# Kernel optimization log

Measured on AMD Instinct MI355X. Metric: run time of the kernel, lower is better.

## Reference

```python
import jax, jax.numpy as jnp
import numpy as np

V, E, H, B, S, T = 32000, 512, 1024, 64, 128, 65

def setup_inputs() -> dict:
    key = jax.random.key(0)
    ks = jax.random.split(key, 10)
    f = lambda k, shape, s=1.0: jax.random.normal(k, shape, jnp.float32) * s
    return {
        "tgt_token_ids": jax.random.randint(ks[0], (T, B), 0, V),
        "enc_hidden": f(ks[1], (B, S, 2 * H)),
        "enc_mask": jnp.zeros((B, S), jnp.int32),  # 1 = masked (pad)
        "dec_init_hidden": f(ks[2], (B, H)),
        "dec_init_cell": f(ks[3], (B, H)),
        "embedding": f(ks[4], (V, E), 0.02),
        "W_ih": f(ks[5], (4 * H, E + H), 0.02),
        "W_hh": f(ks[6], (4 * H, H), 0.02),
        "b_ih": jnp.zeros((4 * H,), jnp.float32),
        "b_hh": jnp.zeros((4 * H,), jnp.float32),
        "W_att": f(ks[7], (H, 2 * H), 0.02),
        "W_comb": f(ks[8], (H, 3 * H), 0.02),
    }


def reference(tgt_token_ids, enc_hidden, enc_mask, dec_init_hidden, dec_init_cell,
              embedding, W_ih, W_hh, b_ih, b_hh, W_att, W_comb):
    mask = enc_mask.astype(bool)
    # enc_hiddens_proj = attention(enc_hidden): [B,S,2H] @ [H,2H].T -> [B,S,H]
    enc_proj = jnp.einsum('bsd,hd->bsh', enc_hidden, W_att)
    y = embedding[tgt_token_ids[:-1]]  # [T-1, B, E]
    # NOTE: faithful to the source, dec_init_state is fed to step() at EVERY
    # timestep (the updated LSTM state is discarded); only o_prev recurs.
    hh_term = dec_init_hidden @ W_hh.T + b_ih + b_hh  # [B, 4H], constant across steps
    c0 = dec_init_cell

    def step(o_prev, y_t):
        ybar = jnp.concatenate([y_t, o_prev], axis=1)        # [B, E+H]
        gates = ybar @ W_ih.T + hh_term                      # [B, 4H]
        i, f, g, o = jnp.split(gates, 4, axis=1)
        c = jax.nn.sigmoid(f) * c0 + jax.nn.sigmoid(i) * jnp.tanh(g)
        h = jax.nn.sigmoid(o) * jnp.tanh(c)                  # dec_hidden [B, H]
        e = jnp.einsum('bsh,bh->bs', enc_proj, h)            # scores [B, S]
        e = jnp.where(mask, -jnp.inf, e)
        alpha = jax.nn.softmax(e, axis=1)
        a = jnp.einsum('bs,bsd->bd', alpha, enc_hidden)      # context [B, 2H]
        U = jnp.concatenate([h, a], axis=1)                  # [B, 3H]
        O = jnp.tanh(U @ W_comb.T)                           # [B, H] (dropout = identity, eval)
        return O, O

    o0 = jnp.zeros_like(dec_init_hidden)
    _, outs = jax.lax.scan(step, o0, y)                      # [T-1, B, H]
    return outs
```

## Files before the change

kernel.cpp:

```cpp
#include <hip/hip_runtime.h>
#include <hip/hip_bf16.h>
#include <math.h>

#define BATCH 64
#define SRC   128
#define HID   1024
#define EMB   512
#define NT    64
#define G4    4096

__device__ __forceinline__ float sigmoidf_(float x){ return 1.0f/(1.0f+expf(-x)); }

template<int AMODE>
__launch_bounds__(256, 2)
__global__ void skinny_gemm(const float* __restrict__ A, int lda,
                            const int* __restrict__ toks, const float* __restrict__ emb,
                            const float* __restrict__ W, int ldw,
                            float* __restrict__ partial, int N, int Kchunk){
  const int nc = blockIdx.x;
  const int kc = blockIdx.y;
  const int kbase = kc * Kchunk;
  const int tid = threadIdx.x;
  __shared__ float As[16][68];
  __shared__ float Bs[16][132];
  const int wave = tid >> 6, lane = tid & 63;
  const int lm = lane & 7, ln = lane >> 3;
  const int nwave = nc*128 + wave*32;
  float acc[8][4] = {};
  const int arow = tid >> 2, akc = (tid & 3) * 4;
  for (int k0 = 0; k0 < Kchunk; k0 += 16){
    int kg = kbase + k0 + akc;
    float4 av;
    if (AMODE == 1){
      if (kg < EMB) av = *(const float4*)(emb + (size_t)toks[arow]*EMB + kg);
      else          av = *(const float4*)(A + (size_t)arow*lda + (kg - EMB));
    } else {
      av = *(const float4*)(A + (size_t)arow*lda + kg);
    }
    As[akc+0][arow]=av.x; As[akc+1][arow]=av.y; As[akc+2][arow]=av.z; As[akc+3][arow]=av.w;
    #pragma unroll
    for (int r = 0; r < 2; ++r){
      int idx = tid + r*256;
      int nrow = idx >> 2, bkc = (idx & 3) * 4;
      float4 wv = *(const float4*)(W + (size_t)(nc*128 + nrow)*ldw + kbase + k0 + bkc);
      Bs[bkc+0][nrow]=wv.x; Bs[bkc+1][nrow]=wv.y; Bs[bkc+2][nrow]=wv.z; Bs[bkc+3][nrow]=wv.w;
    }
    __syncthreads();
    #pragma unroll
    for (int k = 0; k < 16; ++k){
      float4 alo = *(const float4*)&As[k][lm*8];
      float4 ahi = *(const float4*)&As[k][lm*8+4];
      float4 b4  = *(const float4*)&Bs[k][wave*32 + ln*4];
      float am[8] = {alo.x,alo.y,alo.z,alo.w,ahi.x,ahi.y,ahi.z,ahi.w};
      float bn[4] = {b4.x,b4.y,b4.z,b4.w};
      #pragma unroll
      for (int i=0;i<8;++i)
        #pragma unroll
        for (int j=0;j<4;++j)
          acc[i][j] += am[i]*bn[j];
    }
    __syncthreads();
  }
  for (int i=0;i<8;++i){
    int m = lm*8+i;
    float4 v = make_float4(acc[i][0],acc[i][1],acc[i][2],acc[i][3]);
    *(float4*)(partial + ((size_t)(kc*64 + m))*N + nwave + ln*4) = v;
  }
}

__launch_bounds__(256, 2)
__global__ void big_gemm128(const float* __restrict__ A, int lda,
                            const float* __restrict__ W, int ldw,
                            float* __restrict__ C, int N, int K){
  const int n0 = blockIdx.x * 128;
  const int m0 = blockIdx.y * 128;
  const int tid = threadIdx.x;
  __shared__ float As[16][132];
  __shared__ float Bs[16][132];
  const int wave = tid >> 6, lane = tid & 63;
  const int wm = wave >> 1, wn = wave & 1;
  const int lm = lane & 7, ln = lane >> 3;
  float acc[8][8] = {};
  for (int k0 = 0; k0 < K; k0 += 16){
    #pragma unroll
    for (int r = 0; r < 2; ++r){
      int idx = tid + r*256;
      int row = idx >> 2, kq = (idx & 3) * 4;
      float4 av = *(const float4*)(A + (size_t)(m0+row)*lda + k0 + kq);
      As[kq+0][row]=av.x; As[kq+1][row]=av.y; As[kq+2][row]=av.z; As[kq+3][row]=av.w;
      float4 wv = *(const float4*)(W + (size_t)(n0+row)*ldw + k0 + kq);
      Bs[kq+0][row]=wv.x; Bs[kq+1][row]=wv.y; Bs[kq+2][row]=wv.z; Bs[kq+3][row]=wv.w;
    }
    __syncthreads();
    #pragma unroll
    for (int k = 0; k < 16; ++k){
      float4 a0 = *(const float4*)&As[k][wm*64 + lm*8];
      float4 a1 = *(const float4*)&As[k][wm*64 + lm*8 + 4];
      float4 b0 = *(const float4*)&Bs[k][wn*64 + ln*8];
      float4 b1 = *(const float4*)&Bs[k][wn*64 + ln*8 + 4];
      float am[8] = {a0.x,a0.y,a0.z,a0.w,a1.x,a1.y,a1.z,a1.w};
      float bn[8] = {b0.x,b0.y,b0.z,b0.w,b1.x,b1.y,b1.z,b1.w};
      #pragma unroll
      for (int i=0;i<8;++i)
        #pragma unroll
        for (int j=0;j<8;++j)
          acc[i][j] += am[i]*bn[j];
    }
    __syncthreads();
  }
  for (int i=0;i<8;++i){
    int m = m0 + wm*64 + lm*8 + i;
    float* cp = C + (size_t)m*N + n0 + wn*64 + ln*8;
    *(float4*)cp     = make_float4(acc[i][0],acc[i][1],acc[i][2],acc[i][3]);
    *(float4*)(cp+4) = make_float4(acc[i][4],acc[i][5],acc[i][6],acc[i][7]);
  }
}

__global__ void hh_reduce_kernel(const float* __restrict__ partial,
                                 const float* __restrict__ b_ih, const float* __restrict__ b_hh,
                                 float* __restrict__ hh_term){
  int g = blockIdx.x*512 + threadIdx.x;
  int n = g & 4095;
  int b = g >> 12;
  float s = b_ih[n] + b_hh[n];
  #pragma unroll
  for (int kc=0; kc<8; ++kc) s += partial[((size_t)(kc*64+b))*G4 + n];
  hh_term[g] = s;
}

__global__ void h_e_kernel(const float* __restrict__ partial_g, const float* __restrict__ hh_term,
                           const float* __restrict__ c0, const float* __restrict__ enc_proj,
                           float* __restrict__ hbuf, float* __restrict__ e_part){
  const int b = blockIdx.x, ch = blockIdx.y;
  const int tid = threadIdx.x;
  __shared__ float hs[256];
  const int j = ch*256 + tid;
  float gate[4];
  #pragma unroll
  for (int q=0;q<4;++q){
    int n = q*HID + j;
    float s = hh_term[b*G4 + n];
    #pragma unroll
    for (int kc=0;kc<8;++kc) s += partial_g[((size_t)(kc*64+b))*G4 + n];
    gate[q]=s;
  }
  float c = sigmoidf_(gate[1])*c0[b*HID+j] + sigmoidf_(gate[0])*tanhf(gate[2]);
  float h = sigmoidf_(gate[3])*tanhf(c);
  hs[tid] = h;
  hbuf[b*HID + j] = h;
  __syncthreads();
  const int wave = tid>>6, lane = tid&63;
  float4 hv = *(const float4*)&hs[lane*4];
  for (int s = wave; s < SRC; s += 4){
    const float* ep = enc_proj + ((size_t)b*SRC + s)*HID + ch*256;
    float4 v = *(const float4*)(ep + lane*4);
    float sum = v.x*hv.x + v.y*hv.y + v.z*hv.z + v.w*hv.w;
    #pragma unroll
    for (int off=32; off; off>>=1) sum += __shfl_down(sum, off);
    if (lane==0) e_part[(b*4 + ch)*SRC + s] = sum;
  }
}

__global__ void soft_comb_kernel(const float* __restrict__ e_part, const int* __restrict__ enc_mask,
                                 const float* __restrict__ encW, const float* __restrict__ partial_c,
                                 float* __restrict__ Obuf, float* __restrict__ out, int t){
  const int b = blockIdx.x, ch = blockIdx.y;
  const int tid = threadIdx.x;
  __shared__ float als[SRC];
  __shared__ float red[SRC];
  float ev = 0.f; bool msk = false;
  if (tid < SRC){
    ev = e_part[(b*4+0)*SRC+tid] + e_part[(b*4+1)*SRC+tid]
       + e_part[(b*4+2)*SRC+tid] + e_part[(b*4+3)*SRC+tid];
    msk = (enc_mask[b*SRC+tid] != 0);
    red[tid] = msk ? -1e30f : ev;
  }
  __syncthreads();
  for (int off=64; off>=1; off>>=1){ if (tid<off) red[tid]=fmaxf(red[tid],red[tid+off]); __syncthreads(); }
  float mval = red[0]; __syncthreads();
  float p = (tid<SRC && !msk) ? expf(ev-mval) : 0.f;
  if (tid<SRC) red[tid]=p;
  __syncthreads();
  for (int off=64; off>=1; off>>=1){ if (tid<off) red[tid]+=red[tid+off]; __syncthreads(); }
  if (tid<SRC) als[tid] = p/red[0];
  __syncthreads();
  const int j = ch*256 + tid;
  const float* ew = encW + (size_t)b*SRC*HID + j;
  float acc = 0.f;
  #pragma unroll 8
  for (int s=0;s<SRC;++s) acc += als[s]*ew[(size_t)s*HID];
  #pragma unroll
  for (int kc=0;kc<16;++kc) acc += partial_c[((size_t)(kc*64+b))*HID + j];
  float v = tanhf(acc);
  Obuf[b*HID+j] = v;
  out[(size_t)t*BATCH*HID + b*HID + j] = v;
}

__global__ void zero_kernel(float* __restrict__ p, int n){
  int i = blockIdx.x*256 + threadIdx.x;
  if (i < n) p[i] = 0.f;
}

extern "C" void kernel_launch(void* const* d_in, const int* in_sizes, int n_in,
                              void* d_out, int out_size, void* d_ws, size_t ws_size,
                              hipStream_t stream) {
  const int*   tgt        = (const int*)d_in[0];
  const float* enc_hidden = (const float*)d_in[1];
  const int*   enc_mask   = (const int*)d_in[2];
  const float* dih        = (const float*)d_in[3];
  const float* dic        = (const float*)d_in[4];
  const float* emb        = (const float*)d_in[5];
  const float* W_ih       = (const float*)d_in[6];
  const float* W_hh       = (const float*)d_in[7];
  const float* b_ih       = (const float*)d_in[8];
  const float* b_hh       = (const float*)d_in[9];
  const float* W_att      = (const float*)d_in[10];
  const float* W_comb     = (const float*)d_in[11];
  float* out = (float*)d_out;

  float* ws        = (float*)d_ws;
  float* enc_proj  = ws;
  float* encW      = enc_proj + 8388608;
  float* partial_g = encW + 8388608;
  float* partial_c = partial_g + 2097152;
  float* hh_term   = partial_c + 1048576;
  float* hbuf      = hh_term + 262144;
  float* e_part    = hbuf + 65536;
  float* Obuf      = e_part + 32768;

  big_gemm128<<<dim3(8,64), 256, 0, stream>>>(enc_hidden, 2048, W_att, 2048, enc_proj, HID, 2048);
  big_gemm128<<<dim3(8,64), 256, 0, stream>>>(enc_hidden, 2048, W_comb + HID, 3072, encW, HID, 2048);
  skinny_gemm<0><<<dim3(32,8), 256, 0, stream>>>(dih, HID, nullptr, nullptr, W_hh, HID, partial_g, G4, 128);
  hh_reduce_kernel<<<dim3(512), 512, 0, stream>>>(partial_g, b_ih, b_hh, hh_term);
  zero_kernel<<<dim3(256), 256, 0, stream>>>(Obuf, BATCH*HID);

  for (int t = 0; t < NT; ++t){
    skinny_gemm<1><<<dim3(32,8), 256, 0, stream>>>(Obuf, HID, tgt + t*BATCH, emb, W_ih, 1536, partial_g, G4, 192);
    h_e_kernel<<<dim3(64,4), 256, 0, stream>>>(partial_g, hh_term, dic, enc_proj, hbuf, e_part);
    skinny_gemm<0><<<dim3(8,16), 256, 0, stream>>>(hbuf, HID, nullptr, nullptr, W_comb, 3072, partial_c, HID, 64);
    soft_comb_kernel<<<dim3(64,4), 256, 0, stream>>>(e_part, enc_mask, encW, partial_c, Obuf, out, t);
  }
}
```

Before: 5.166 ms.

## Replace per-timestep kernel launches with a persistent decoder using grid barriers

The 64-step loop of four kernels per step becomes one persistent kernel of 256 blocks. Each block keeps its slice of W_ih and W_comb resident in shared memory and steps through time, separated by software grid barriers built on atomics. The aim is to remove launch overhead and the repeated re-reading of weights from global memory on every step. It risks deadlock if the 256 blocks are not all co-resident, since each uses a large shared memory allocation, and it adds barrier latency and a split-softmax combine.

```diff
diff --git a/kernel.cpp b/kernel.cpp
--- a/kernel.cpp
+++ b/kernel.cpp
@@ -128,77 +128,232 @@
   hh_term[g] = s;
 }
 
-__global__ void h_e_kernel(const float* __restrict__ partial_g, const float* __restrict__ hh_term,
-                           const float* __restrict__ c0, const float* __restrict__ enc_proj,
-                           float* __restrict__ hbuf, float* __restrict__ e_part){
-  const int b = blockIdx.x, ch = blockIdx.y;
-  const int tid = threadIdx.x;
-  __shared__ float hs[256];
-  const int j = ch*256 + tid;
-  float gate[4];
-  #pragma unroll
-  for (int q=0;q<4;++q){
-    int n = q*HID + j;
-    float s = hh_term[b*G4 + n];
-    #pragma unroll
-    for (int kc=0;kc<8;++kc) s += partial_g[((size_t)(kc*64+b))*G4 + n];
-    gate[q]=s;
-  }
-  float c = sigmoidf_(gate[1])*c0[b*HID+j] + sigmoidf_(gate[0])*tanhf(gate[2]);
-  float h = sigmoidf_(gate[3])*tanhf(c);
-  hs[tid] = h;
-  hbuf[b*HID + j] = h;
+__global__ void init_kernel(float* __restrict__ Obuf, unsigned* __restrict__ bar){
+  int i = blockIdx.x*512 + threadIdx.x;
+  if (i < BATCH*HID) Obuf[i] = 0.f;
+  if (i < 4) bar[i] = 0u;
+}
+
+__device__ __forceinline__ void grid_barrier(unsigned* bar, unsigned nblocks){
   __syncthreads();
-  const int wave = tid>>6, lane = tid&63;
-  float4 hv = *(const float4*)&hs[lane*4];
-  for (int s = wave; s < SRC; s += 4){
-    const float* ep = enc_proj + ((size_t)b*SRC + s)*HID + ch*256;
-    float4 v = *(const float4*)(ep + lane*4);
-    float sum = v.x*hv.x + v.y*hv.y + v.z*hv.z + v.w*hv.w;
-    #pragma unroll
-    for (int off=32; off; off>>=1) sum += __shfl_down(sum, off);
-    if (lane==0) e_part[(b*4 + ch)*SRC + s] = sum;
-  }
-}
-
-__global__ void soft_comb_kernel(const float* __restrict__ e_part, const int* __restrict__ enc_mask,
-                                 const float* __restrict__ encW, const float* __restrict__ partial_c,
-                                 float* __restrict__ Obuf, float* __restrict__ out, int t){
-  const int b = blockIdx.x, ch = blockIdx.y;
-  const int tid = threadIdx.x;
-  __shared__ float als[SRC];
-  __shared__ float red[SRC];
-  float ev = 0.f; bool msk = false;
-  if (tid < SRC){
-    ev = e_part[(b*4+0)*SRC+tid] + e_part[(b*4+1)*SRC+tid]
-       + e_part[(b*4+2)*SRC+tid] + e_part[(b*4+3)*SRC+tid];
-    msk = (enc_mask[b*SRC+tid] != 0);
-    red[tid] = msk ? -1e30f : ev;
+  if (threadIdx.x == 0){
+    __threadfence();
+    unsigned g = __hip_atomic_load(&bar[1], __ATOMIC_ACQUIRE, __HIP_MEMORY_SCOPE_AGENT);
+    unsigned old = __hip_atomic_fetch_add(&bar[0], 1u, __ATOMIC_ACQ_REL, __HIP_MEMORY_SCOPE_AGENT);
+    if (old == nblocks - 1u){
+      __hip_atomic_store(&bar[0], 0u, __ATOMIC_RELAXED, __HIP_MEMORY_SCOPE_AGENT);
+      __threadfence();
+      __hip_atomic_fetch_add(&bar[1], 1u, __ATOMIC_ACQ_REL, __HIP_MEMORY_SCOPE_AGENT);
+    } else {
+      while (__hip_atomic_load(&bar[1], __ATOMIC_ACQUIRE, __HIP_MEMORY_SCOPE_AGENT) == g)
+        __builtin_amdgcn_s_sleep(2);
+    }
+    __threadfence();
   }
   __syncthreads();
-  for (int off=64; off>=1; off>>=1){ if (tid<off) red[tid]=fmaxf(red[tid],red[tid+off]); __syncthreads(); }
-  float mval = red[0]; __syncthreads();
-  float p = (tid<SRC && !msk) ? expf(ev-mval) : 0.f;
-  if (tid<SRC) red[tid]=p;
+}
+
+__global__ __launch_bounds__(512, 1)
+void decoder_persistent(const int* __restrict__ tgt, const int* __restrict__ enc_mask,
+                        const float* __restrict__ dic, const float* __restrict__ emb,
+                        const float* __restrict__ W_ih, const float* __restrict__ W_comb,
+                        const float* __restrict__ hh_term, const float* __restrict__ enc_proj,
+                        const float* __restrict__ encW,
+                        float* __restrict__ e_g, float* __restrict__ emax_g, float* __restrict__ esum_g,
+                        float* __restrict__ combh, float* __restrict__ hbuf,
+                        float* __restrict__ Obuf, float* __restrict__ out,
+                        unsigned* __restrict__ bar){
+  const int blk = blockIdx.x, tid = threadIdx.x;
+  const int wave = tid >> 6, lane = tid & 63;
+  const int bg = lane >> 2, rg = lane & 3;
+  const int j0 = blk * 4;
+
+  __shared__ float Wg[1536*16];
+  __shared__ float Wc[1024*4];
+  __shared__ float scratch[8704];
+  __shared__ int   toks[64];
+  __shared__ float e_loc[32];
+  __shared__ float al_s[SRC];
+  __shared__ float redp[512];
+
+  for (int rr = 0; rr < 16; ++rr){
+    int row = (rr & 3) * 1024 + j0 + (rr >> 2);
+    for (int k = tid; k < 1536; k += 512) Wg[k*16 + rr] = W_ih[(size_t)row*1536 + k];
+  }
+  for (int j = 0; j < 4; ++j){
+    int n = j0 + j;
+    for (int k = tid; k < 1024; k += 512) Wc[k*4 + j] = W_comb[(size_t)n*3072 + k];
+  }
   __syncthreads();
-  for (int off=64; off>=1; off>>=1){ if (tid<off) red[tid]+=red[tid+off]; __syncthreads(); }
-  if (tid<SRC) als[tid] = p/red[0];
-  __syncthreads();
-  const int j = ch*256 + tid;
-  const float* ew = encW + (size_t)b*SRC*HID + j;
-  float acc = 0.f;
-  #pragma unroll 8
-  for (int s=0;s<SRC;++s) acc += als[s]*ew[(size_t)s*HID];
-  #pragma unroll
-  for (int kc=0;kc<16;++kc) acc += partial_c[((size_t)(kc*64+b))*HID + j];
-  float v = tanhf(acc);
-  Obuf[b*HID+j] = v;
-  out[(size_t)t*BATCH*HID + b*HID + j] = v;
-}
-
-__global__ void zero_kernel(float* __restrict__ p, int n){
-  int i = blockIdx.x*256 + threadIdx.x;
-  if (i < n) p[i] = 0.f;
+
+  for (int t = 0; t < NT; ++t){
+    if (tid < 64) toks[tid] = tgt[t*BATCH + tid];
+    __syncthreads();
+    float acc[4][4] = {};
+    for (int c = 0; c < 12; ++c){
+      {
+        int b = tid & 63, kq = tid >> 6;
+        #pragma unroll
+        for (int i = 0; i < 4; ++i){
+          int kg = c*128 + kq*16 + i*4;
+          float4 v;
+          if (kg < EMB) v = *(const float4*)(emb + (size_t)toks[b]*EMB + kg);
+          else          v = *(const float4*)(Obuf + b*HID + (kg - EMB));
+          int kb = kq*16 + i*4;
+          scratch[(kb+0)*68 + b] = v.x;
+          scratch[(kb+1)*68 + b] = v.y;
+          scratch[(kb+2)*68 + b] = v.z;
+          scratch[(kb+3)*68 + b] = v.w;
+        }
+      }
+      __syncthreads();
+      #pragma unroll
+      for (int kk = 0; kk < 16; ++kk){
+        int k = wave*16 + kk;
+        float4 yb = *(const float4*)&scratch[k*68 + bg*4];
+        float4 wv = *(const float4*)&Wg[(c*128 + k)*16 + rg*4];
+        float ym[4] = {yb.x, yb.y, yb.z, yb.w};
+        float wn[4] = {wv.x, wv.y, wv.z, wv.w};
+        #pragma unroll
+        for (int i = 0; i < 4; ++i)
+          #pragma unroll
+          for (int j = 0; j < 4; ++j)
+            acc[i][j] += ym[i] * wn[j];
+      }
+      __syncthreads();
+    }
+    #pragma unroll
+    for (int i = 0; i < 4; ++i)
+      #pragma unroll
+      for (int j = 0; j < 4; ++j)
+        scratch[wave*1024 + (rg*4 + j)*64 + bg*4 + i] = acc[i][j];
+    __syncthreads();
+    if (tid < 256){
+      int b = tid & 63, jj = tid >> 6;
+      float g4[4];
+      #pragma unroll
+      for (int g = 0; g < 4; ++g){
+        float s = hh_term[b*G4 + g*1024 + j0 + jj];
+        #pragma unroll
+        for (int w = 0; w < 8; ++w) s += scratch[w*1024 + (jj*4 + g)*64 + b];
+        g4[g] = s;
+      }
+      float c_ = sigmoidf_(g4[1]) * dic[b*HID + j0 + jj] + sigmoidf_(g4[0]) * tanhf(g4[2]);
+      hbuf[b*HID + j0 + jj] = sigmoidf_(g4[3]) * tanhf(c_);
+    }
+    grid_barrier(bar, 256);
+
+    {
+      const int b = blk >> 2, sg = blk & 3;
+      for (int i = tid; i < HID; i += 512) scratch[i] = hbuf[b*HID + i];
+      __syncthreads();
+      #pragma unroll
+      for (int q = 0; q < 4; ++q){
+        int s = sg*32 + wave*4 + q;
+        const float* ep = enc_proj + ((size_t)(b*SRC + s))*HID;
+        float sum = 0.f;
+        #pragma unroll
+        for (int m = 0; m < 4; ++m){
+          float4 v  = *(const float4*)(ep + m*256 + lane*4);
+          float4 hv = *(const float4*)&scratch[m*256 + lane*4];
+          sum += v.x*hv.x + v.y*hv.y + v.z*hv.z + v.w*hv.w;
+        }
+        #pragma unroll
+        for (int off = 32; off; off >>= 1) sum += __shfl_down(sum, off);
+        if (lane == 0) e_loc[wave*4 + q] = sum;
+      }
+      __syncthreads();
+      if (wave == 0){
+        int sl = lane & 31;
+        int s = sg*32 + sl;
+        bool valid = lane < 32;
+        bool msk = valid ? (enc_mask[b*SRC + s] != 0) : true;
+        float ev = (valid && !msk) ? e_loc[sl] : -1e30f;
+        if (valid) e_g[b*SRC + s] = ev;
+        float mv = ev;
+        #pragma unroll
+        for (int off = 32; off; off >>= 1) mv = fmaxf(mv, __shfl_down(mv, off));
+        mv = __shfl(mv, 0);
+        float p = (valid && !msk) ? expf(ev - mv) : 0.f;
+        float ps = p;
+        #pragma unroll
+        for (int off = 32; off; off >>= 1) ps += __shfl_down(ps, off);
+        if (lane == 0){ emax_g[b*4 + sg] = mv; esum_g[b*4 + sg] = ps; }
+      }
+      __syncthreads();
+    }
+    {
+      float acc2[4] = {0.f, 0.f, 0.f, 0.f};
+      for (int c = 0; c < 8; ++c){
+        {
+          int b = tid & 63, kq = tid >> 6;
+          #pragma unroll
+          for (int i = 0; i < 4; ++i){
+            int kg = c*128 + kq*16 + i*4;
+            float4 v = *(const float4*)(hbuf + b*HID + kg);
+            int kb = kq*16 + i*4;
+            scratch[(kb+0)*68 + b] = v.x;
+            scratch[(kb+1)*68 + b] = v.y;
+            scratch[(kb+2)*68 + b] = v.z;
+            scratch[(kb+3)*68 + b] = v.w;
+          }
+        }
+        __syncthreads();
+        #pragma unroll
+        for (int kk = 0; kk < 16; ++kk){
+          int k = wave*16 + kk;
+          float4 hb = *(const float4*)&scratch[k*68 + bg*4];
+          float w  = Wc[(c*128 + k)*4 + rg];
+          acc2[0] += hb.x * w; acc2[1] += hb.y * w;
+          acc2[2] += hb.z * w; acc2[3] += hb.w * w;
+        }
+        __syncthreads();
+      }
+      #pragma unroll
+      for (int i = 0; i < 4; ++i)
+        scratch[wave*256 + rg*64 + bg*4 + i] = acc2[i];
+      __syncthreads();
+      if (tid < 256){
+        int b = tid & 63, j = tid >> 6;
+        float s = 0.f;
+        #pragma unroll
+        for (int w = 0; w < 8; ++w) s += scratch[w*256 + j*64 + b];
+        combh[b*HID + j0 + j] = s;
+      }
+    }
+    grid_barrier(bar, 256);
+
+    {
+      const int b = blk >> 2, nq = blk & 3;
+      if (wave == 0){
+        float m0_ = fmaxf(fmaxf(emax_g[b*4+0], emax_g[b*4+1]), fmaxf(emax_g[b*4+2], emax_g[b*4+3]));
+        float Z = 0.f;
+        #pragma unroll
+        for (int sgi = 0; sgi < 4; ++sgi) Z += expf(emax_g[b*4+sgi] - m0_) * esum_g[b*4+sgi];
+        #pragma unroll
+        for (int rep = 0; rep < 2; ++rep){
+          int s = rep*64 + lane;
+          al_s[s] = expf(e_g[b*SRC + s] - m0_) / Z;
+        }
+      }
+      __syncthreads();
+      int n = nq*256 + (tid & 255), sh = tid >> 8;
+      const float* ew = encW + ((size_t)(b*SRC + sh*64))*HID + n;
+      float a_ = 0.f;
+      #pragma unroll 8
+      for (int s = 0; s < 64; ++s) a_ += al_s[sh*64 + s] * ew[(size_t)s*HID];
+      redp[tid] = a_;
+      __syncthreads();
+      if (tid < 256){
+        int nn = nq*256 + tid;
+        float v = redp[tid] + redp[tid + 256] + combh[b*HID + nn];
+        v = tanhf(v);
+        out[((size_t)t*BATCH + b)*HID + nn] = v;
+        Obuf[b*HID + nn] = v;
+      }
+    }
+    grid_barrier(bar, 256);
+  }
 }
 
 extern "C" void kernel_launch(void* const* d_in, const int* in_sizes, int n_in,
@@ -221,23 +376,23 @@
   float* ws        = (float*)d_ws;
   float* enc_proj  = ws;
   float* encW      = enc_proj + 8388608;
-  float* partial_g = encW + 8388608;
-  float* partial_c = partial_g + 2097152;
-  float* hh_term   = partial_c + 1048576;
+  float* pg        = encW + 8388608;
+  float* hh_term   = pg + 2097152;
   float* hbuf      = hh_term + 262144;
-  float* e_part    = hbuf + 65536;
-  float* Obuf      = e_part + 32768;
+  float* e_g       = hbuf + 65536;
+  float* emax_g    = e_g + 8192;
+  float* esum_g    = emax_g + 256;
+  float* combh     = esum_g + 256;
+  float* Obuf      = combh + 65536;
+  unsigned* bar    = (unsigned*)(Obuf + 65536);
 
   big_gemm128<<<dim3(8,64), 256, 0, stream>>>(enc_hidden, 2048, W_att, 2048, enc_proj, HID, 2048);
   big_gemm128<<<dim3(8,64), 256, 0, stream>>>(enc_hidden, 2048, W_comb + HID, 3072, encW, HID, 2048);
-  skinny_gemm<0><<<dim3(32,8), 256, 0, stream>>>(dih, HID, nullptr, nullptr, W_hh, HID, partial_g, G4, 128);
-  hh_reduce_kernel<<<dim3(512), 512, 0, stream>>>(partial_g, b_ih, b_hh, hh_term);
-  zero_kernel<<<dim3(256), 256, 0, stream>>>(Obuf, BATCH*HID);
-
-  for (int t = 0; t < NT; ++t){
-    skinny_gemm<1><<<dim3(32,8), 256, 0, stream>>>(Obuf, HID, tgt + t*BATCH, emb, W_ih, 1536, partial_g, G4, 192);
-    h_e_kernel<<<dim3(64,4), 256, 0, stream>>>(partial_g, hh_term, dic, enc_proj, hbuf, e_part);
-    skinny_gemm<0><<<dim3(8,16), 256, 0, stream>>>(hbuf, HID, nullptr, nullptr, W_comb, 3072, partial_c, HID, 64);
-    soft_comb_kernel<<<dim3(64,4), 256, 0, stream>>>(e_part, enc_mask, encW, partial_c, Obuf, out, t);
-  }
-}
+  skinny_gemm<0><<<dim3(32,8), 256, 0, stream>>>(dih, HID, nullptr, nullptr, W_hh, HID, pg, G4, 128);
+  hh_reduce_kernel<<<dim3(512), 512, 0, stream>>>(pg, b_ih, b_hh, hh_term);
+  init_kernel<<<dim3(128), 512, 0, stream>>>(Obuf, bar);
+
+  decoder_persistent<<<dim3(256), 512, 0, stream>>>(
+      tgt, enc_mask, dic, emb, W_ih, W_comb, hh_term, enc_proj, encW,
+      e_g, emax_g, esum_g, combh, hbuf, Obuf, out, bar);
+}
```

Measured after the change: 13.17 ms. +155.0%, slower.

## Fuse per-step LSTM gates, hidden update and attention scores into one kernel

Applied to the files above, without the earlier changes.

Each timestep now runs two kernels instead of four. The first computes the full-K gate GEMM per block against a pre-packed W_ih, then applies the LSTM cell and the attention-score partials in place, which removes the split-K partial buffers and their reductions. The second fuses the softmax, the h@W_comb projection (using a pre-transposed W_comb) and the context combination. It reads the previous output directly from the output tensor, so no separate Obuf is kept. The trade-offs are fewer, larger blocks (256 and 256) with less K-parallelism, and an e_part reduction over 256 slices in the second kernel.

```diff
diff --git a/kernel.cpp b/kernel.cpp
--- a/kernel.cpp
+++ b/kernel.cpp
@@ -11,10 +11,8 @@
 
 __device__ __forceinline__ float sigmoidf_(float x){ return 1.0f/(1.0f+expf(-x)); }
 
-template<int AMODE>
 __launch_bounds__(256, 2)
 __global__ void skinny_gemm(const float* __restrict__ A, int lda,
-                            const int* __restrict__ toks, const float* __restrict__ emb,
                             const float* __restrict__ W, int ldw,
                             float* __restrict__ partial, int N, int Kchunk){
   const int nc = blockIdx.x;
@@ -30,13 +28,7 @@
   const int arow = tid >> 2, akc = (tid & 3) * 4;
   for (int k0 = 0; k0 < Kchunk; k0 += 16){
     int kg = kbase + k0 + akc;
-    float4 av;
-    if (AMODE == 1){
-      if (kg < EMB) av = *(const float4*)(emb + (size_t)toks[arow]*EMB + kg);
-      else          av = *(const float4*)(A + (size_t)arow*lda + (kg - EMB));
-    } else {
-      av = *(const float4*)(A + (size_t)arow*lda + kg);
-    }
+    float4 av = *(const float4*)(A + (size_t)arow*lda + kg);
     As[akc+0][arow]=av.x; As[akc+1][arow]=av.y; As[akc+2][arow]=av.z; As[akc+3][arow]=av.w;
     #pragma unroll
     for (int r = 0; r < 2; ++r){
@@ -128,77 +120,177 @@
   hh_term[g] = s;
 }
 
-__global__ void h_e_kernel(const float* __restrict__ partial_g, const float* __restrict__ hh_term,
-                           const float* __restrict__ c0, const float* __restrict__ enc_proj,
-                           float* __restrict__ hbuf, float* __restrict__ e_part){
-  const int b = blockIdx.x, ch = blockIdx.y;
+__global__ void transpose_wc(const float* __restrict__ W_comb, float* __restrict__ WcT){
+  __shared__ float tile[32][33];
+  int bx = blockIdx.x, by = blockIdx.y;
+  int tx = threadIdx.x & 31, ty = threadIdx.x >> 5;
+  int j0 = by*32, k0 = bx*32;
+  #pragma unroll
+  for (int r = 0; r < 4; ++r)
+    tile[ty + r*8][tx] = W_comb[(size_t)(j0 + ty + r*8)*3072 + k0 + tx];
+  __syncthreads();
+  #pragma unroll
+  for (int r = 0; r < 4; ++r)
+    WcT[(size_t)(k0 + ty + r*8)*1024 + j0 + tx] = tile[tx][ty + r*8];
+}
+
+__global__ void pack_wih(const float* __restrict__ W_ih, float* __restrict__ Wgp){
+  int blk = blockIdx.x;
+  int tid = threadIdx.x;
+  for (int rr = 0; rr < 16; ++rr){
+    int row = (rr & 3)*1024 + blk*4 + (rr >> 2);
+    for (int k = tid; k < 1536; k += 256)
+      Wgp[((size_t)blk*1536 + k)*16 + rr] = W_ih[(size_t)row*1536 + k];
+  }
+}
+
+__global__ void init_kernel(float* __restrict__ O0){
+  int i = blockIdx.x*512 + threadIdx.x;
+  if (i < BATCH*HID) O0[i] = 0.f;
+}
+
+__global__ __launch_bounds__(512, 1)
+void k1_gates_h_epart(const int* __restrict__ tgt, int t,
+                      const float* __restrict__ emb, const float* __restrict__ Oprev,
+                      const float* __restrict__ Wgp, const float* __restrict__ hh_term,
+                      const float* __restrict__ dic, const float* __restrict__ enc_proj,
+                      float* __restrict__ hbuf, float* __restrict__ e_part){
+  const int blk = blockIdx.x, tid = threadIdx.x;
+  const int wave = tid >> 6, lane = tid & 63;
+  const int bg = lane >> 2, rg = lane & 3;
+  const int j0 = blk * 4;
+  const float* wgp = Wgp + (size_t)blk*1536*16;
+
+  __shared__ float scratch[8704];
+  __shared__ float hs[64][4];
+  __shared__ int   toks[64];
+
+  if (tid < 64) toks[tid] = tgt[t*BATCH + tid];
+  __syncthreads();
+
+  float acc[4][4] = {};
+  for (int c = 0; c < 12; ++c){
+    {
+      int b = tid & 63, kq = tid >> 6;
+      #pragma unroll
+      for (int i = 0; i < 4; ++i){
+        int kg = c*128 + kq*16 + i*4;
+        float4 v;
+        if (kg < EMB) v = *(const float4*)(emb + (size_t)toks[b]*EMB + kg);
+        else          v = *(const float4*)(Oprev + b*HID + (kg - EMB));
+        int kb = kq*16 + i*4;
+        scratch[(kb+0)*68 + b] = v.x;
+        scratch[(kb+1)*68 + b] = v.y;
+        scratch[(kb+2)*68 + b] = v.z;
+        scratch[(kb+3)*68 + b] = v.w;
+      }
+    }
+    __syncthreads();
+    #pragma unroll
+    for (int kk = 0; kk < 16; ++kk){
+      int k = wave*16 + kk;
+      float4 yb = *(const float4*)&scratch[k*68 + bg*4];
+      float4 wv = *(const float4*)(wgp + (size_t)(c*128 + k)*16 + rg*4);
+      float ym[4] = {yb.x, yb.y, yb.z, yb.w};
+      float wn[4] = {wv.x, wv.y, wv.z, wv.w};
+      #pragma unroll
+      for (int i = 0; i < 4; ++i)
+        #pragma unroll
+        for (int j = 0; j < 4; ++j)
+          acc[i][j] += ym[i] * wn[j];
+    }
+    __syncthreads();
+  }
+  #pragma unroll
+  for (int i = 0; i < 4; ++i)
+    #pragma unroll
+    for (int j = 0; j < 4; ++j)
+      scratch[wave*1024 + (rg*4 + j)*64 + bg*4 + i] = acc[i][j];
+  __syncthreads();
+  if (tid < 256){
+    int b = tid & 63, jj = tid >> 6;
+    float g4[4];
+    #pragma unroll
+    for (int g = 0; g < 4; ++g){
+      float s = hh_term[b*G4 + g*1024 + j0 + jj];
+      #pragma unroll
+      for (int w = 0; w < 8; ++w) s += scratch[w*1024 + (jj*4 + g)*64 + b];
+      g4[g] = s;
+    }
+    float c_ = sigmoidf_(g4[1]) * dic[b*HID + j0 + jj] + sigmoidf_(g4[0]) * tanhf(g4[2]);
+    float h = sigmoidf_(g4[3]) * tanhf(c_);
+    hbuf[b*HID + j0 + jj] = h;
+    hs[b][jj] = h;
+  }
+  __syncthreads();
+  for (int idx = tid; idx < BATCH*SRC; idx += 512){
+    int b = idx >> 7, s = idx & 127;
+    float4 ep = *(const float4*)(enc_proj + ((size_t)(b*SRC + s))*HID + j0);
+    float4 hv = *(const float4*)&hs[b][0];
+    e_part[(size_t)blk*BATCH*SRC + idx] = ep.x*hv.x + ep.y*hv.y + ep.z*hv.z + ep.w*hv.w;
+  }
+}
+
+__global__ __launch_bounds__(512, 1)
+void k2_soft_comb(const float* __restrict__ e_part, const int* __restrict__ enc_mask,
+                  const float* __restrict__ hbuf, const float* __restrict__ WcT,
+                  const float* __restrict__ encW, float* __restrict__ out, int t){
+  const int b = blockIdx.x, nq = blockIdx.y;
   const int tid = threadIdx.x;
-  __shared__ float hs[256];
-  const int j = ch*256 + tid;
-  float gate[4];
-  #pragma unroll
-  for (int q=0;q<4;++q){
-    int n = q*HID + j;
-    float s = hh_term[b*G4 + n];
-    #pragma unroll
-    for (int kc=0;kc<8;++kc) s += partial_g[((size_t)(kc*64+b))*G4 + n];
-    gate[q]=s;
-  }
-  float c = sigmoidf_(gate[1])*c0[b*HID+j] + sigmoidf_(gate[0])*tanhf(gate[2]);
-  float h = sigmoidf_(gate[3])*tanhf(c);
-  hs[tid] = h;
-  hbuf[b*HID + j] = h;
-  __syncthreads();
-  const int wave = tid>>6, lane = tid&63;
-  float4 hv = *(const float4*)&hs[lane*4];
-  for (int s = wave; s < SRC; s += 4){
-    const float* ep = enc_proj + ((size_t)b*SRC + s)*HID + ch*256;
-    float4 v = *(const float4*)(ep + lane*4);
-    float sum = v.x*hv.x + v.y*hv.y + v.z*hv.z + v.w*hv.w;
-    #pragma unroll
-    for (int off=32; off; off>>=1) sum += __shfl_down(sum, off);
-    if (lane==0) e_part[(b*4 + ch)*SRC + s] = sum;
-  }
-}
-
-__global__ void soft_comb_kernel(const float* __restrict__ e_part, const int* __restrict__ enc_mask,
-                                 const float* __restrict__ encW, const float* __restrict__ partial_c,
-                                 float* __restrict__ Obuf, float* __restrict__ out, int t){
-  const int b = blockIdx.x, ch = blockIdx.y;
-  const int tid = threadIdx.x;
-  __shared__ float als[SRC];
+  __shared__ float hsh[HID];
+  __shared__ float er[4][SRC];
   __shared__ float red[SRC];
-  float ev = 0.f; bool msk = false;
+  __shared__ float al_s[SRC];
+  __shared__ float ch[2][256];
+
+  for (int i = tid; i < HID; i += 512) hsh[i] = hbuf[b*HID + i];
+
+  {
+    int s = tid & 127, g = tid >> 7;
+    const float* epb = e_part + (size_t)g*64*BATCH*SRC + b*SRC + s;
+    float sum = 0.f;
+    #pragma unroll 8
+    for (int i = 0; i < 64; ++i) sum += epb[(size_t)i*BATCH*SRC];
+    er[g][s] = sum;
+  }
+  __syncthreads();
+  float ev = -1e30f;
   if (tid < SRC){
-    ev = e_part[(b*4+0)*SRC+tid] + e_part[(b*4+1)*SRC+tid]
-       + e_part[(b*4+2)*SRC+tid] + e_part[(b*4+3)*SRC+tid];
-    msk = (enc_mask[b*SRC+tid] != 0);
-    red[tid] = msk ? -1e30f : ev;
+    ev = er[0][tid] + er[1][tid] + er[2][tid] + er[3][tid];
+    if (enc_mask[b*SRC + tid] != 0) ev = -1e30f;
+    red[tid] = ev;
   }
   __syncthreads();
   for (int off=64; off>=1; off>>=1){ if (tid<off) red[tid]=fmaxf(red[tid],red[tid+off]); __syncthreads(); }
   float mval = red[0]; __syncthreads();
-  float p = (tid<SRC && !msk) ? expf(ev-mval) : 0.f;
-  if (tid<SRC) red[tid]=p;
+  float p = (tid < SRC) ? expf(ev - mval) : 0.f;
+  if (tid < SRC) red[tid] = p;
   __syncthreads();
   for (int off=64; off>=1; off>>=1){ if (tid<off) red[tid]+=red[tid+off]; __syncthreads(); }
-  if (tid<SRC) als[tid] = p/red[0];
-  __syncthreads();
-  const int j = ch*256 + tid;
-  const float* ew = encW + (size_t)b*SRC*HID + j;
-  float acc = 0.f;
-  #pragma unroll 8
-  for (int s=0;s<SRC;++s) acc += als[s]*ew[(size_t)s*HID];
-  #pragma unroll
-  for (int kc=0;kc<16;++kc) acc += partial_c[((size_t)(kc*64+b))*HID + j];
-  float v = tanhf(acc);
-  Obuf[b*HID+j] = v;
-  out[(size_t)t*BATCH*HID + b*HID + j] = v;
-}
-
-__global__ void zero_kernel(float* __restrict__ p, int n){
-  int i = blockIdx.x*256 + threadIdx.x;
-  if (i < n) p[i] = 0.f;
+  if (tid < SRC) al_s[tid] = p / red[0];
+  __syncthreads();
+
+  {
+    int jc = tid & 255, kh = tid >> 8;
+    int j = nq*256 + jc;
+    const float* wct = WcT + (size_t)(kh*512)*HID + j;
+    const float* hp  = &hsh[kh*512];
+    float acc = 0.f;
+    #pragma unroll 8
+    for (int k = 0; k < 512; ++k) acc += hp[k] * wct[(size_t)k*HID];
+    ch[kh][jc] = acc;
+  }
+  __syncthreads();
+
+  if (tid < 256){
+    int j = nq*256 + tid;
+    const float* ew = encW + (size_t)b*SRC*HID + j;
+    float a_ = 0.f;
+    #pragma unroll 8
+    for (int s = 0; s < SRC; ++s) a_ += al_s[s] * ew[(size_t)s*HID];
+    float v = tanhf(a_ + ch[0][tid] + ch[1][tid]);
+    out[((size_t)t*BATCH + b)*HID + j] = v;
+  }
 }
 
 extern "C" void kernel_launch(void* const* d_in, const int* in_sizes, int n_in,
@@ -221,23 +313,27 @@
   float* ws        = (float*)d_ws;
   float* enc_proj  = ws;
   float* encW      = enc_proj + 8388608;
-  float* partial_g = encW + 8388608;
-  float* partial_c = partial_g + 2097152;
-  float* hh_term   = partial_c + 1048576;
-  float* hbuf      = hh_term + 262144;
-  float* e_part    = hbuf + 65536;
-  float* Obuf      = e_part + 32768;
+  float* hh_term   = encW + 8388608;
+  float* WcT       = hh_term + 262144;
+  float* Wgp       = WcT + 1048576;
+  float* e_part    = Wgp + 6291456;
+  float* hbuf      = e_part + 2097152;
+  float* O0        = hbuf + 65536;
+  float* pg        = e_part;
 
   big_gemm128<<<dim3(8,64), 256, 0, stream>>>(enc_hidden, 2048, W_att, 2048, enc_proj, HID, 2048);
   big_gemm128<<<dim3(8,64), 256, 0, stream>>>(enc_hidden, 2048, W_comb + HID, 3072, encW, HID, 2048);
-  skinny_gemm<0><<<dim3(32,8), 256, 0, stream>>>(dih, HID, nullptr, nullptr, W_hh, HID, partial_g, G4, 128);
-  hh_reduce_kernel<<<dim3(512), 512, 0, stream>>>(partial_g, b_ih, b_hh, hh_term);
-  zero_kernel<<<dim3(256), 256, 0, stream>>>(Obuf, BATCH*HID);
+  skinny_gemm<<<dim3(32,8), 256, 0, stream>>>(dih, HID, W_hh, HID, pg, G4, 128);
+  hh_reduce_kernel<<<dim3(512), 512, 0, stream>>>(pg, b_ih, b_hh, hh_term);
+  transpose_wc<<<dim3(32,32), 256, 0, stream>>>(W_comb, WcT);
+  pack_wih<<<dim3(256), 256, 0, stream>>>(W_ih, Wgp);
+  init_kernel<<<dim3(128), 512, 0, stream>>>(O0);
 
   for (int t = 0; t < NT; ++t){
-    skinny_gemm<1><<<dim3(32,8), 256, 0, stream>>>(Obuf, HID, tgt + t*BATCH, emb, W_ih, 1536, partial_g, G4, 192);
-    h_e_kernel<<<dim3(64,4), 256, 0, stream>>>(partial_g, hh_term, dic, enc_proj, hbuf, e_part);
-    skinny_gemm<0><<<dim3(8,16), 256, 0, stream>>>(hbuf, HID, nullptr, nullptr, W_comb, 3072, partial_c, HID, 64);
-    soft_comb_kernel<<<dim3(64,4), 256, 0, stream>>>(e_part, enc_mask, encW, partial_c, Obuf, out, t);
-  }
-}
+    const float* Oprev = (t == 0) ? O0 : out + (size_t)(t-1)*BATCH*HID;
+    k1_gates_h_epart<<<dim3(256), 512, 0, stream>>>(
+        tgt, t, emb, Oprev, Wgp, hh_term, dic, enc_proj, hbuf, e_part);
+    k2_soft_comb<<<dim3(64,4), 512, 0, stream>>>(
+        e_part, enc_mask, hbuf, WcT, encW, out, t);
+  }
+}
```

After: 10.34 ms. 2x slower.
